# Performance work log

Hardware: AMD Instinct MI355X
Metric: run time of the kernel (lower is better)

## Reference

```python
import jax, jax.numpy as jnp
import numpy as np

N_INT4, N_INT8, K, GROUP = 6144, 2048, 8192, 128
N_TOTAL = N_INT4 + N_INT8
M = 16


def setup_inputs() -> dict:
    key = jax.random.key(0)
    ks = jax.random.split(key, 8)
    x = jax.random.normal(ks[0], (M, K), jnp.float32)
    # uint4 weights: values 0..15 (stored int32)
    w_int4 = jax.random.randint(ks[1], (N_INT4, K), 0, 16, jnp.int32)
    # group-wise scales [N_int4, K//group_size]
    s_int4 = jax.random.uniform(ks[2], (N_INT4, K // GROUP), jnp.float32, minval=0.005, maxval=0.02)
    # int8 weights stored in offset-128 form (w_int8 + 128 -> 0..255), as pack_for_marlin builds
    w_uint8 = jax.random.randint(ks[3], (N_INT8, K), 0, 256, jnp.int32)
    # per-channel int8 scales
    s_int8 = jax.random.uniform(ks[4], (N_INT8,), jnp.float32, minval=0.005, maxval=0.02)
    awq_scales = jax.random.uniform(ks[5], (K,), jnp.float32, minval=0.5, maxval=2.0)
    bias = jax.random.normal(ks[6], (N_TOTAL,), jnp.float32) * 0.01
    inv_perm = jax.random.permutation(ks[7], N_TOTAL).astype(jnp.int32)
    return dict(x=x, w_int4=w_int4, s_int4=s_int4, w_uint8=w_uint8, s_int8=s_int8,
                awq_scales=awq_scales, bias=bias, inv_perm=inv_perm, group_size=GROUP)


def reference(x, w_int4, s_int4, w_uint8, s_int8, awq_scales, bias, inv_perm, group_size):
    dt = x.dtype
    k = x.shape[-1]
    # AWQ input scaling (unfused path: x / awq_scales)
    x2 = x.reshape(-1, k) / awq_scales[None, :]
    sum_x = jnp.sum(x2, axis=1, keepdims=True)  # [M, 1]

    # Marlin uint4b8 dequant: (q - 8) * scale, group-wise scales for int4 rows
    s4_k = jnp.repeat(s_int4, group_size, axis=1)            # [N4, K]
    W4 = (w_int4.astype(dt) - 8.0) * s4_k                    # [N4, K]

    # int8 rows split into high/low nibbles with scales 16*s and s
    high = (w_uint8 >> 4) & 15
    low = w_uint8 & 15
    Wh = (high.astype(dt) - 8.0) * (16.0 * s_int8)[:, None]  # [N8, K]
    Wl = (low.astype(dt) - 8.0) * s_int8[:, None]            # [N8, K]

    Wc = jnp.concatenate([W4, Wh, Wl], axis=0)               # [N4+2*N8, K]
    y = x2 @ Wc.T                                            # marlin_gemm equivalent

    n4 = W4.shape[0]
    n8 = s_int8.shape[0]
    y4 = y[:, :n4]
    # int8 reconstruction: y_high + y_low + 8*s_int8*sum_x  == s_int8 * (x @ w_int8^T)
    y8 = y[:, n4:n4 + n8] + y[:, n4 + n8:] + (8.0 * s_int8)[None, :] * sum_x
    y_out = jnp.concatenate([y4, y8], axis=-1)[:, inv_perm] + bias[None, :]
    return y_out.reshape(*x.shape[:-1], n4 + n8)
```

## Files before the change

kernel.cpp:

```cpp
#include <hip/hip_runtime.h>
#include <hip/hip_bf16.h>

constexpr int K    = 8192;
constexpr int N4   = 6144;
constexpr int N8   = 2048;
constexpr int NT   = N4 + N8;
constexpr int NG   = K / 128;
constexpr int KS   = 4096;

typedef short  short8  __attribute__((ext_vector_type(8)));
typedef float  floatx4 __attribute__((ext_vector_type(4)));
typedef int    intx4   __attribute__((ext_vector_type(4)));

__device__ inline short f2bf(float f) {
    __hip_bfloat16 h = __float2bfloat16(f);
    return __builtin_bit_cast(short, h);
}

__global__ void prep_kernel(const float* __restrict__ x,
                            const float* __restrict__ awq,
                            const int*   __restrict__ inv_perm,
                            const float* __restrict__ bias,
                            short* __restrict__ x2bf,
                            int*   __restrict__ fwd,
                            float* __restrict__ out) {
    const int tid  = blockIdx.x * blockDim.x + threadIdx.x;
    const int c    = tid >> 9;
    const int rem  = tid & 511;
    const int lane = rem >> 3;
    const int j    = rem & 7;
    const int m    = lane & 15;
    const int k    = c * 32 + (lane >> 4) * 8 + j;
    x2bf[tid] = f2bf(x[m * K + k] / awq[k]);
    if (tid < NT) fwd[inv_perm[tid]] = tid;
    out[tid] = bias[tid & (NT - 1)];
}

__global__ __launch_bounds__(256, 4)
void qgemv_kernel(const short* __restrict__ xf,
                  const int*   __restrict__ w4,
                  const float* __restrict__ s4,
                  const int*   __restrict__ w8,
                  const float* __restrict__ s8,
                  const int*   __restrict__ fwd,
                  float* __restrict__ out) {
    __shared__ float lds[4 * 256];

    const int t     = threadIdx.x;
    const int lane  = t & 63;
    const int w     = t >> 6;
    const int tile  = blockIdx.x >> 1;
    const int split = blockIdx.x & 1;
    const int nb    = tile * 16;
    const int i     = lane & 15;
    const int q     = lane >> 4;
    const int row   = nb + i;

    const bool is4  = (nb < N4);
    const int kbase = split * KS + w * 1024;
    const int*   wp = (is4 ? (w4 + (size_t)row * K)
                           : (w8 + (size_t)(row - N4) * K))
                      + kbase + q * 8;
    const short* xw = xf + (size_t)(kbase >> 5) * 512 + lane * 8;
    const float* sp = is4 ? (s4 + (size_t)row * NG + (kbase >> 7)) : nullptr;

    floatx4 acc = {0.f, 0.f, 0.f, 0.f};

    intx4  wbA[8], wbB[8];
    short8 abA[4], abB[4];
    float  sA = 0.f, sB = 0.f;

    auto loadg = [&](int g, intx4* wb, short8* ab, float& s) {
        #pragma unroll
        for (int c = 0; c < 4; ++c) {
            const size_t co = (size_t)(g * 4 + c);
            wb[2 * c]     = __builtin_nontemporal_load((const intx4*)(wp + co * 32));
            wb[2 * c + 1] = __builtin_nontemporal_load((const intx4*)(wp + co * 32 + 4));
            ab[c]         = *(const short8*)(xw + co * 512);
        }
        if (is4) s = sp[g];
    };

    auto compg = [&](const intx4* wb, const short8* ab, float s) {
        const float sc = is4 ? s : 1.f;
        const float sb = is4 ? -8.f * s : -128.f;
        #pragma unroll
        for (int c = 0; c < 4; ++c) {
            const intx4 wa = wb[2 * c];
            const intx4 wz = wb[2 * c + 1];
            short8 bf;
            bf[0] = f2bf((float)wa[0] * sc + sb);
            bf[1] = f2bf((float)wa[1] * sc + sb);
            bf[2] = f2bf((float)wa[2] * sc + sb);
            bf[3] = f2bf((float)wa[3] * sc + sb);
            bf[4] = f2bf((float)wz[0] * sc + sb);
            bf[5] = f2bf((float)wz[1] * sc + sb);
            bf[6] = f2bf((float)wz[2] * sc + sb);
            bf[7] = f2bf((float)wz[3] * sc + sb);
            acc = __builtin_amdgcn_mfma_f32_16x16x32_bf16(ab[c], bf, acc, 0, 0, 0);
        }
    };

    loadg(0, wbA, abA, sA);
    __builtin_amdgcn_sched_barrier(0);
    #pragma unroll 1
    for (int g = 0; g < 6; g += 2) {
        loadg(g + 1, wbB, abB, sB);
        __builtin_amdgcn_sched_barrier(0);
        compg(wbA, abA, sA);
        loadg(g + 2, wbA, abA, sA);
        __builtin_amdgcn_sched_barrier(0);
        compg(wbB, abB, sB);
    }
    loadg(7, wbB, abB, sB);
    __builtin_amdgcn_sched_barrier(0);
    compg(wbA, abA, sA);
    compg(wbB, abB, sB);

    #pragma unroll
    for (int r = 0; r < 4; ++r)
        lds[w * 256 + (q * 4 + r) * 16 + i] = acc[r];
    __syncthreads();

    {
        const int m  = t >> 4;
        const int i2 = t & 15;
        const float v = lds[0 * 256 + t] + lds[1 * 256 + t]
                      + lds[2 * 256 + t] + lds[3 * 256 + t];
        const int n  = nb + i2;
        const float sc = is4 ? 1.f : s8[n - N4];
        const int d  = fwd[n];
        atomicAdd(&out[(size_t)m * NT + d], v * sc);
    }
}

extern "C" void kernel_launch(void* const* d_in, const int* in_sizes, int n_in,
                              void* d_out, int out_size, void* d_ws, size_t ws_size,
                              hipStream_t stream) {
    const float* x        = (const float*)d_in[0];
    const int*   w_int4   = (const int*)  d_in[1];
    const float* s_int4   = (const float*)d_in[2];
    const int*   w_uint8  = (const int*)  d_in[3];
    const float* s_int8   = (const float*)d_in[4];
    const float* awq      = (const float*)d_in[5];
    const float* bias     = (const float*)d_in[6];
    const int*   inv_perm = (const int*)  d_in[7];

    short* x2bf = (short*)d_ws;
    int*   fwd  = (int*)((char*)d_ws + (size_t)16 * K * sizeof(short));

    prep_kernel<<<(16 * K) / 256, 256, 0, stream>>>(x, awq, inv_perm, bias,
                                                    x2bf, fwd, (float*)d_out);
    qgemv_kernel<<<(NT / 16) * 2, 256, 0, stream>>>(x2bf, w_int4, s_int4,
                                                    w_uint8, s_int8, fwd,
                                                    (float*)d_out);
}
```

Baseline: 330.6 us.

## Process two 16-row tiles per block to reuse activation loads

Each block now covers 32 output rows instead of 16, keeping two MFMA accumulators that share the same activation fragment. The grid is halved and each block loops over twice as many k-steps, so the bf16 x reads per weight byte drop by half. The launch-bounds occupancy hint is removed, which can raise register use and lower waves per CU. Fewer blocks (512) may also underfill the GPU for a weight-bandwidth-bound GEMV.

Result: no change. 330.8 us (+0.0%).

```diff
diff --git a/kernel.cpp b/kernel.cpp
--- a/kernel.cpp
+++ b/kernel.cpp
@@ -36,7 +36,7 @@
     out[tid] = bias[tid & (NT - 1)];
 }
 
-__global__ __launch_bounds__(256, 4)
+__global__ __launch_bounds__(256)
 void qgemv_kernel(const short* __restrict__ xf,
                   const int*   __restrict__ w4,
                   const float* __restrict__ s4,
@@ -44,93 +44,109 @@
                   const float* __restrict__ s8,
                   const int*   __restrict__ fwd,
                   float* __restrict__ out) {
-    __shared__ float lds[4 * 256];
+    __shared__ float lds[4 * 512];
 
     const int t     = threadIdx.x;
     const int lane  = t & 63;
     const int w     = t >> 6;
     const int tile  = blockIdx.x >> 1;
     const int split = blockIdx.x & 1;
-    const int nb    = tile * 16;
+    const int nb    = tile * 32;
     const int i     = lane & 15;
     const int q     = lane >> 4;
-    const int row   = nb + i;
+    const int rlo   = nb + i;
+    const int rhi   = nb + 16 + i;
 
     const bool is4  = (nb < N4);
     const int kbase = split * KS + w * 1024;
-    const int*   wp = (is4 ? (w4 + (size_t)row * K)
-                           : (w8 + (size_t)(row - N4) * K))
-                      + kbase + q * 8;
+    const int* wplo = (is4 ? (w4 + (size_t)rlo * K)
+                           : (w8 + (size_t)(rlo - N4) * K)) + kbase + q * 8;
+    const int* wphi = (is4 ? (w4 + (size_t)rhi * K)
+                           : (w8 + (size_t)(rhi - N4) * K)) + kbase + q * 8;
     const short* xw = xf + (size_t)(kbase >> 5) * 512 + lane * 8;
-    const float* sp = is4 ? (s4 + (size_t)row * NG + (kbase >> 7)) : nullptr;
+    const float* splo = is4 ? (s4 + (size_t)rlo * NG + (kbase >> 7)) : nullptr;
+    const float* sphi = is4 ? (s4 + (size_t)rhi * NG + (kbase >> 7)) : nullptr;
 
-    floatx4 acc = {0.f, 0.f, 0.f, 0.f};
+    floatx4 accL = {0.f, 0.f, 0.f, 0.f};
+    floatx4 accH = {0.f, 0.f, 0.f, 0.f};
 
     intx4  wbA[8], wbB[8];
-    short8 abA[4], abB[4];
-    float  sA = 0.f, sB = 0.f;
+    short8 xA[2], xB[2];
+    float  sLA = 0.f, sHA = 0.f, sLB = 0.f, sHB = 0.f;
 
-    auto loadg = [&](int g, intx4* wb, short8* ab, float& s) {
+    auto loadg = [&](int g, intx4* wb, short8* xv, float& sL, float& sH) {
         #pragma unroll
-        for (int c = 0; c < 4; ++c) {
-            const size_t co = (size_t)(g * 4 + c);
-            wb[2 * c]     = __builtin_nontemporal_load((const intx4*)(wp + co * 32));
-            wb[2 * c + 1] = __builtin_nontemporal_load((const intx4*)(wp + co * 32 + 4));
-            ab[c]         = *(const short8*)(xw + co * 512);
+        for (int c = 0; c < 2; ++c) {
+            const size_t co = (size_t)(g * 2 + c);
+            wb[4 * c]     = __builtin_nontemporal_load((const intx4*)(wplo + co * 32));
+            wb[4 * c + 1] = __builtin_nontemporal_load((const intx4*)(wplo + co * 32 + 4));
+            wb[4 * c + 2] = __builtin_nontemporal_load((const intx4*)(wphi + co * 32));
+            wb[4 * c + 3] = __builtin_nontemporal_load((const intx4*)(wphi + co * 32 + 4));
+            xv[c]         = *(const short8*)(xw + co * 512);
         }
-        if (is4) s = sp[g];
+        if (is4) { sL = splo[g >> 1]; sH = sphi[g >> 1]; }
     };
 
-    auto compg = [&](const intx4* wb, const short8* ab, float s) {
-        const float sc = is4 ? s : 1.f;
-        const float sb = is4 ? -8.f * s : -128.f;
+    auto dq8 = [&](const intx4& a, const intx4& z, float sc, float sb) {
+        short8 bf;
+        bf[0] = f2bf((float)a[0] * sc + sb);
+        bf[1] = f2bf((float)a[1] * sc + sb);
+        bf[2] = f2bf((float)a[2] * sc + sb);
+        bf[3] = f2bf((float)a[3] * sc + sb);
+        bf[4] = f2bf((float)z[0] * sc + sb);
+        bf[5] = f2bf((float)z[1] * sc + sb);
+        bf[6] = f2bf((float)z[2] * sc + sb);
+        bf[7] = f2bf((float)z[3] * sc + sb);
+        return bf;
+    };
+
+    auto compg = [&](const intx4* wb, const short8* xv, float sL, float sH) {
+        const float scL = is4 ? sL : 1.f, sbL = is4 ? -8.f * sL : -128.f;
+        const float scH = is4 ? sH : 1.f, sbH = is4 ? -8.f * sH : -128.f;
         #pragma unroll
-        for (int c = 0; c < 4; ++c) {
-            const intx4 wa = wb[2 * c];
-            const intx4 wz = wb[2 * c + 1];
-            short8 bf;
-            bf[0] = f2bf((float)wa[0] * sc + sb);
-            bf[1] = f2bf((float)wa[1] * sc + sb);
-            bf[2] = f2bf((float)wa[2] * sc + sb);
-            bf[3] = f2bf((float)wa[3] * sc + sb);
-            bf[4] = f2bf((float)wz[0] * sc + sb);
-            bf[5] = f2bf((float)wz[1] * sc + sb);
-            bf[6] = f2bf((float)wz[2] * sc + sb);
-            bf[7] = f2bf((float)wz[3] * sc + sb);
-            acc = __builtin_amdgcn_mfma_f32_16x16x32_bf16(ab[c], bf, acc, 0, 0, 0);
+        for (int c = 0; c < 2; ++c) {
+            const short8 bfL = dq8(wb[4 * c],     wb[4 * c + 1], scL, sbL);
+            accL = __builtin_amdgcn_mfma_f32_16x16x32_bf16(xv[c], bfL, accL, 0, 0, 0);
+            const short8 bfH = dq8(wb[4 * c + 2], wb[4 * c + 3], scH, sbH);
+            accH = __builtin_amdgcn_mfma_f32_16x16x32_bf16(xv[c], bfH, accH, 0, 0, 0);
         }
     };
 
-    loadg(0, wbA, abA, sA);
+    loadg(0, wbA, xA, sLA, sHA);
     __builtin_amdgcn_sched_barrier(0);
     #pragma unroll 1
-    for (int g = 0; g < 6; g += 2) {
-        loadg(g + 1, wbB, abB, sB);
+    for (int g = 0; g < 14; g += 2) {
+        loadg(g + 1, wbB, xB, sLB, sHB);
         __builtin_amdgcn_sched_barrier(0);
-        compg(wbA, abA, sA);
-        loadg(g + 2, wbA, abA, sA);
+        compg(wbA, xA, sLA, sHA);
+        loadg(g + 2, wbA, xA, sLA, sHA);
         __builtin_amdgcn_sched_barrier(0);
-        compg(wbB, abB, sB);
+        compg(wbB, xB, sLB, sHB);
     }
-    loadg(7, wbB, abB, sB);
+    loadg(15, wbB, xB, sLB, sHB);
     __builtin_amdgcn_sched_barrier(0);
-    compg(wbA, abA, sA);
-    compg(wbB, abB, sB);
+    compg(wbA, xA, sLA, sHA);
+    compg(wbB, xB, sLB, sHB);
 
     #pragma unroll
-    for (int r = 0; r < 4; ++r)
-        lds[w * 256 + (q * 4 + r) * 16 + i] = acc[r];
+    for (int r = 0; r < 4; ++r) {
+        lds[w * 512 +       (q * 4 + r) * 16 + i] = accL[r];
+        lds[w * 512 + 256 + (q * 4 + r) * 16 + i] = accH[r];
+    }
     __syncthreads();
 
     {
         const int m  = t >> 4;
         const int i2 = t & 15;
-        const float v = lds[0 * 256 + t] + lds[1 * 256 + t]
-                      + lds[2 * 256 + t] + lds[3 * 256 + t];
-        const int n  = nb + i2;
-        const float sc = is4 ? 1.f : s8[n - N4];
-        const int d  = fwd[n];
-        atomicAdd(&out[(size_t)m * NT + d], v * sc);
+        #pragma unroll
+        for (int h = 0; h < 2; ++h) {
+            const float v = lds[0 * 512 + h * 256 + t] + lds[1 * 512 + h * 256 + t]
+                          + lds[2 * 512 + h * 256 + t] + lds[3 * 512 + h * 256 + t];
+            const int n  = nb + h * 16 + i2;
+            const float sc = is4 ? 1.f : s8[n - N4];
+            const int d  = fwd[n];
+            atomicAdd(&out[(size_t)m * NT + d], v * sc);
+        }
     }
 }
 
@@ -151,7 +167,7 @@
 
     prep_kernel<<<(16 * K) / 256, 256, 0, stream>>>(x, awq, inv_perm, bias,
                                                     x2bf, fwd, (float*)d_out);
-    qgemv_kernel<<<(NT / 16) * 2, 256, 0, stream>>>(x2bf, w_int4, s_int4,
+    qgemv_kernel<<<(NT / 32) * 2, 256, 0, stream>>>(x2bf, w_int4, s_int4,
                                                     w_uint8, s_int8, fwd,
                                                     (float*)d_out);
 }
```
